# Kernel tuning notes

Measured on AMD Instinct MI355X. Metric: run time of the kernel, lower is better.

The kernel has to match this reference:

```python
import jax, jax.numpy as jnp
import numpy as np

NUM_HEADS = 8


def _forward(x, Wq, bq, Wk, bk, Wv, bv, Wo, bo, w1, b1, w2, b2, tau):
    B, S, E = x.shape
    H = NUM_HEADS
    hd = E // H
    scale = hd ** -0.5

    def heads(t):
        return t.reshape(B, S, H, hd).transpose(0, 2, 1, 3)  # [B,H,S,hd]

    q = heads(x @ Wq + bq)
    k = heads(x @ Wk + bk)
    v = heads(x @ Wv + bv)
    s = jnp.einsum('bhqd,bhkd->bhqk', q, k) * scale  # [B,H,S,S]

    # ---- autopoietic transform (vectorized over batch, no mask) ----
    s = jnp.clip(jnp.nan_to_num(s, nan=0.0, posinf=10.0, neginf=-10.0), -15.0, 15.0)
    ma = s.mean(axis=1)  # mean over heads -> [B,S,S]
    eps_safe = 0.05  # clamp(eps=1e-6, 0.05, 0.8)
    sa = jnp.clip(jnp.clip(ma, -8.0, 8.0) * eps_safe, -10.0, 10.0)
    # 1x1 conv on [1,1,S,S] == per-channel scalar scale+bias -> [B,C,S,S]
    hid = jax.nn.relu(jnp.clip(sa[:, None] * w1[None, :, None, None]
                               + b1[None, :, None, None], -5.0, 5.0))
    ap = jnp.clip(jnp.einsum('bcij,c->bij', hid, w2) + b2, -5.0, 5.0)
    taylor = jnp.clip(1.0 + 0.05 * (ap * 50.0), 0.5, 1.5)
    sig = jax.nn.sigmoid(taylor)
    p = jax.nn.softmax(jnp.clip(ma, -10.0, 10.0), axis=-1)
    Hent = -p * jnp.log(p + 1e-6)
    Fm = jax.nn.softmax(3.0 * Hent, axis=-1)
    t = sig * Fm
    eo = jnp.sqrt((ma * ma).sum(axis=(1, 2), keepdims=True)) + 1e-4  # fro norm
    et = jnp.sqrt((t * t).sum(axis=(1, 2), keepdims=True)) + 1e-4
    t = jnp.clip(eo / et, 0.8, 1.2) * t
    tm = t.mean(axis=(1, 2), keepdims=True)
    om = ma.mean(axis=(1, 2), keepdims=True)
    tstd = jnp.sqrt(jnp.clip(((t - tm) ** 2).mean(axis=(1, 2), keepdims=True), 0.01, None))
    ostd = jnp.sqrt(jnp.clip(((ma - om) ** 2).mean(axis=(1, 2), keepdims=True), 0.01, None))
    gd = jnp.clip(ostd / tstd, 0.8, 1.2)
    ar = jnp.clip(jnp.abs(ma).max(axis=(1, 2), keepdims=True), 1.0, 10.0)
    sm = jnp.clip(0.3 / jnp.log1p(ar), 0.1, 0.5)
    st = tm + sm * gd * (t - tm)  # scaled_transform
    ent = Hent.mean(axis=(1, 2), keepdims=True)
    ne = ent / jnp.log(jnp.float32(S))  # normalized entropy (max_entropy = log S)
    rr = 0.4 * (1.0 - jnp.clip(ne, 0.0, 0.4))  # residual ratio (base 0.4, entropy-damped)
    # blend transform back into per-head scores (res_scale = 1.0)
    s = s + rr[:, None] * (st - ma)[:, None]

    attn = jax.nn.softmax(s / tau, axis=-1)
    out = jnp.einsum('bhqk,bhkd->bhqd', attn, v)
    out = out.transpose(0, 2, 1, 3).reshape(B, S, E)
    return out @ Wo + bo


def setup_inputs() -> dict:
    key = jax.random.key(0)
    ks = jax.random.split(key, 8)
    B, S, E, C = 4, 512, 512, 128
    w_scale = 0.02
    return {
        'x': jax.random.normal(ks[0], (B, S, E), dtype=jnp.float32),
        'Wq': jax.random.normal(ks[1], (E, E), dtype=jnp.float32) * w_scale,
        'bq': jnp.zeros((E,), jnp.float32),
        'Wk': jax.random.normal(ks[2], (E, E), dtype=jnp.float32) * w_scale,
        'bk': jnp.zeros((E,), jnp.float32),
        'Wv': jax.random.normal(ks[3], (E, E), dtype=jnp.float32) * w_scale,
        'bv': jnp.zeros((E,), jnp.float32),
        'Wo': jax.random.normal(ks[4], (E, E), dtype=jnp.float32) * w_scale,
        'bo': jnp.zeros((E,), jnp.float32),
        'w1': jax.random.normal(ks[5], (C,), dtype=jnp.float32) * 0.5,
        'b1': jnp.zeros((C,), jnp.float32),
        'w2': jax.random.normal(ks[6], (C,), dtype=jnp.float32) * 0.1,
        'b2': jnp.zeros((1,), jnp.float32),
        'tau': jnp.ones((1,), jnp.float32),
    }


def reference(x, Wq, bq, Wk, bk, Wv, bv, Wo, bo, w1, b1, w2, b2, tau):
    return _forward(x, Wq, bq, Wk, bk, Wv, bv, Wo, bo, w1, b1, w2, b2, tau)
```

## Files before the change

kernel.cpp:

```cpp
#include <hip/hip_runtime.h>
#include <math.h>

#define BB 4
#define SS 512
#define EE 512
#define NH 8
#define HD 64
#define NC 128
#define NTAB 4096

typedef _Float16 f16x8 __attribute__((ext_vector_type(8)));
typedef float f32x4 __attribute__((ext_vector_type(4)));

struct HL { _Float16 h, l; };

__device__ __forceinline__ float clampf(float v, float lo, float hi) {
  return fminf(fmaxf(v, lo), hi);
}
__device__ __forceinline__ HL split16(float x) {
  HL r;
  r.h = (_Float16)x;
  r.l = (_Float16)(x - (float)r.h);
  return r;
}

__device__ __forceinline__ float waveRedSum(float v) {
#pragma unroll
  for (int o = 32; o; o >>= 1) v += __shfl_xor(v, o);
  return v;
}
__device__ __forceinline__ float waveRedMax(float v) {
#pragma unroll
  for (int o = 32; o; o >>= 1) v = fmaxf(v, __shfl_xor(v, o));
  return v;
}
__device__ __forceinline__ float blockRedSum(float v, float* red) {
  int tid = threadIdx.x;
  v = waveRedSum(v);
  __syncthreads();
  if ((tid & 63) == 0) red[tid >> 6] = v;
  __syncthreads();
  return red[0] + red[1] + red[2] + red[3];
}
__device__ __forceinline__ float blockRedMax(float v, float* red) {
  int tid = threadIdx.x;
  v = waveRedMax(v);
  __syncthreads();
  if ((tid & 63) == 0) red[tid >> 6] = v;
  __syncthreads();
  return fmaxf(fmaxf(red[0], red[1]), fmaxf(red[2], red[3]));
}

__global__ __launch_bounds__(256) void k_prep(
    const float* __restrict__ w1, const float* __restrict__ b1,
    const float* __restrict__ w2, const float* __restrict__ b2,
    float* __restrict__ T, const float* __restrict__ x,
    _Float16* __restrict__ xh, _Float16* __restrict__ xl,
    const float* __restrict__ Wq, const float* __restrict__ Wk,
    const float* __restrict__ Wv, const float* __restrict__ Wo,
    _Float16* __restrict__ Wth, _Float16* __restrict__ Wtl) {
  const int bid = blockIdx.x;
  const int tid = threadIdx.x;
  if (bid < 17) {
    int idx = bid * 256 + tid;
    if (idx > NTAB) return;
    float sa = -0.4f + (float)idx * (0.8f / (float)NTAB);
    float ap = 0.f;
#pragma unroll 4
    for (int c = 0; c < NC; ++c) {
      float h = fminf(fmaxf(sa * w1[c] + b1[c], 0.f), 5.f);
      ap += h * w2[c];
    }
    ap = clampf(ap + b2[0], -5.f, 5.f);
    float tay = clampf(1.0f + 0.05f * (ap * 50.0f), 0.5f, 1.5f);
    T[idx] = 1.0f / (1.0f + expf(-tay));
  } else if (bid < 529) {
    int idx = ((bid - 17) * 256 + tid) * 8;
    float4 u0 = *(const float4*)(x + idx);
    float4 u1 = *(const float4*)(x + idx + 4);
    float f[8] = {u0.x, u0.y, u0.z, u0.w, u1.x, u1.y, u1.z, u1.w};
    f16x8 h, l;
#pragma unroll
    for (int j = 0; j < 8; ++j) {
      HL r = split16(f[j]);
      h[j] = r.h;
      l[j] = r.l;
    }
    *(f16x8*)(xh + idx) = h;
    *(f16x8*)(xl + idx) = l;
  } else {
    const int j = bid - 529;
    const int z = j >> 6;
    const int rem = j & 63;
    const int k0 = (rem & 7) * 64, n0 = (rem >> 3) * 64;
    const float* W = (z == 0) ? Wq : (z == 1) ? Wk : (z == 2) ? Wv : Wo;
    __shared__ float Tt[64][68];
    const int r = tid >> 2, c = (tid & 3) * 16;
#pragma unroll
    for (int jj = 0; jj < 16; jj += 4)
      *(float4*)&Tt[r][c + jj] =
          *(const float4*)(W + (size_t)(k0 + r) * EE + n0 + c + jj);
    __syncthreads();
    f16x8 h0, l0, h1, l1;
#pragma unroll
    for (int jj = 0; jj < 8; ++jj) {
      HL r0 = split16(Tt[c + jj][r]);
      HL r1 = split16(Tt[c + 8 + jj][r]);
      h0[jj] = r0.h; l0[jj] = r0.l;
      h1[jj] = r1.h; l1[jj] = r1.l;
    }
    _Float16* dh = Wth + ((size_t)z * EE + n0 + r) * EE + k0 + c;
    _Float16* dl = Wtl + ((size_t)z * EE + n0 + r) * EE + k0 + c;
    *(f16x8*)dh = h0;
    *(f16x8*)(dh + 8) = h1;
    *(f16x8*)dl = l0;
    *(f16x8*)(dl + 8) = l1;
  }
}

__global__ __launch_bounds__(256) void k_qkv_mfma(
    const _Float16* __restrict__ xh, const _Float16* __restrict__ xl,
    const _Float16* __restrict__ Wth, const _Float16* __restrict__ Wtl,
    const float* __restrict__ bq, const float* __restrict__ bk,
    const float* __restrict__ bv,
    _Float16* __restrict__ qh, _Float16* __restrict__ ql,
    _Float16* __restrict__ kh, _Float16* __restrict__ kl,
    _Float16* __restrict__ vth, _Float16* __restrict__ vtl) {
  const int which = blockIdx.z;
  const int tid = threadIdx.x;
  const int wave = tid >> 6, lane = tid & 63;
  const int quad = lane >> 4, l16 = lane & 15;
  const int m0 = blockIdx.y * 64;
  const int n0 = blockIdx.x * 64;
  const _Float16* Bh = Wth + (size_t)which * EE * EE;
  const _Float16* Bl = Wtl + (size_t)which * EE * EE;

  __shared__ __align__(16) char smpool[36864];
  _Float16(*LAh)[72] = (_Float16(*)[72])(smpool);
  _Float16(*LAl)[72] = (_Float16(*)[72])(smpool + 9216);
  _Float16(*LBh)[72] = (_Float16(*)[72])(smpool + 18432);
  _Float16(*LBl)[72] = (_Float16(*)[72])(smpool + 27648);
  float(*TR)[68] = (float(*)[68])(smpool);

  const int sr0 = tid >> 3, sc0 = (tid & 7) * 8;
  const int sr1 = (tid + 256) >> 3, sc1 = sc0;

  f32x4 acc[4] = {};
  for (int k0 = 0; k0 < EE; k0 += 64) {
    if (k0) __syncthreads();
    *(f16x8*)&LAh[sr0][sc0] = *(const f16x8*)(xh + (size_t)(m0 + sr0) * EE + k0 + sc0);
    *(f16x8*)&LAl[sr0][sc0] = *(const f16x8*)(xl + (size_t)(m0 + sr0) * EE + k0 + sc0);
    *(f16x8*)&LBh[sr0][sc0] = *(const f16x8*)(Bh + (size_t)(n0 + sr0) * EE + k0 + sc0);
    *(f16x8*)&LBl[sr0][sc0] = *(const f16x8*)(Bl + (size_t)(n0 + sr0) * EE + k0 + sc0);
    *(f16x8*)&LAh[sr1][sc1] = *(const f16x8*)(xh + (size_t)(m0 + sr1) * EE + k0 + sc1);
    *(f16x8*)&LAl[sr1][sc1] = *(const f16x8*)(xl + (size_t)(m0 + sr1) * EE + k0 + sc1);
    *(f16x8*)&LBh[sr1][sc1] = *(const f16x8*)(Bh + (size_t)(n0 + sr1) * EE + k0 + sc1);
    *(f16x8*)&LBl[sr1][sc1] = *(const f16x8*)(Bl + (size_t)(n0 + sr1) * EE + k0 + sc1);
    __syncthreads();
#pragma unroll
    for (int kk = 0; kk < 64; kk += 32) {
      f16x8 ah = *(const f16x8*)&LAh[wave * 16 + l16][kk + quad * 8];
      f16x8 al = *(const f16x8*)&LAl[wave * 16 + l16][kk + quad * 8];
#pragma unroll
      for (int nt = 0; nt < 4; ++nt) {
        f16x8 bhf = *(const f16x8*)&LBh[nt * 16 + l16][kk + quad * 8];
        f16x8 blf = *(const f16x8*)&LBl[nt * 16 + l16][kk + quad * 8];
        acc[nt] = __builtin_amdgcn_mfma_f32_16x16x32_f16(ah, bhf, acc[nt], 0, 0, 0);
        acc[nt] = __builtin_amdgcn_mfma_f32_16x16x32_f16(ah, blf, acc[nt], 0, 0, 0);
        acc[nt] = __builtin_amdgcn_mfma_f32_16x16x32_f16(al, bhf, acc[nt], 0, 0, 0);
      }
    }
  }
  const float* bias = (which == 0) ? bq : (which == 1) ? bk : bv;
  if (which == 2) {
    __syncthreads();
#pragma unroll
    for (int nt = 0; nt < 4; ++nt) {
      const int dcol = nt * 16 + l16;
      const float bb = bias[n0 + nt * 16 + l16];
#pragma unroll
      for (int r = 0; r < 4; ++r)
        TR[dcol][wave * 16 + quad * 4 + r] = acc[nt][r] + bb;
    }
    __syncthreads();
    const int d = tid >> 2, cc = (tid & 3) * 16;
    const int bh = (m0 >> 9) * NH + (n0 >> 6);
    const int si0 = m0 & 511;
    f16x8 h0, l0, h1, l1;
#pragma unroll
    for (int jj = 0; jj < 8; ++jj) {
      HL r0 = split16(TR[d][cc + jj]);
      HL r1 = split16(TR[d][cc + 8 + jj]);
      h0[jj] = r0.h; l0[jj] = r0.l;
      h1[jj] = r1.h; l1[jj] = r1.l;
    }
    _Float16* dh = vth + ((size_t)bh * HD + d) * SS + si0 + cc;
    _Float16* dl = vtl + ((size_t)bh * HD + d) * SS + si0 + cc;
    *(f16x8*)dh = h0;
    *(f16x8*)(dh + 8) = h1;
    *(f16x8*)dl = l0;
    *(f16x8*)(dl + 8) = l1;
  } else {
    const float postscale = (which == 0) ? 0.125f : 1.0f;
    const int mbase = m0 + wave * 16 + quad * 4;
#pragma unroll
    for (int nt = 0; nt < 4; ++nt) {
      const int col = n0 + nt * 16 + l16;
      const float bb = bias[col];
      const int hh = col >> 6, d = col & 63;
#pragma unroll
      for (int r = 0; r < 4; ++r) {
        const int mm = mbase + r;
        const int b_ = mm >> 9, si = mm & 511;
        const size_t idx = (((size_t)(b_ * NH + hh)) * SS + si) * HD + d;
        const float val = (acc[nt][r] + bb) * postscale;
        HL sp = split16(val);
        (which ? kh : qh)[idx] = sp.h;
        (which ? kl : ql)[idx] = sp.l;
      }
    }
  }
}

__global__ __launch_bounds__(256) void k_scores_mfma(
    const _Float16* __restrict__ qh, const _Float16* __restrict__ ql,
    const _Float16* __restrict__ kh, const _Float16* __restrict__ kl,
    float* __restrict__ s) {
  const int bh = blockIdx.z;
  const int i0 = blockIdx.y * 64, j0 = blockIdx.x * 64;
  const int tid = threadIdx.x;
  const int wave = tid >> 6, lane = tid & 63;
  const int quad = lane >> 4, l16 = lane & 15;

  __shared__ _Float16 Qh[64][72], Ql[64][72], Kh[64][72], Kl[64][72];
  const int r = tid >> 2, c = (tid & 3) * 16;
  {
    const size_t qoff = ((size_t)bh * SS + i0 + r) * HD + c;
    const size_t koff = ((size_t)bh * SS + j0 + r) * HD + c;
    *(f16x8*)&Qh[r][c] = *(const f16x8*)(qh + qoff);
    *(f16x8*)&Qh[r][c + 8] = *(const f16x8*)(qh + qoff + 8);
    *(f16x8*)&Ql[r][c] = *(const f16x8*)(ql + qoff);
    *(f16x8*)&Ql[r][c + 8] = *(const f16x8*)(ql + qoff + 8);
    *(f16x8*)&Kh[r][c] = *(const f16x8*)(kh + koff);
    *(f16x8*)&Kh[r][c + 8] = *(const f16x8*)(kh + koff + 8);
    *(f16x8*)&Kl[r][c] = *(const f16x8*)(kl + koff);
    *(f16x8*)&Kl[r][c + 8] = *(const f16x8*)(kl + koff + 8);
  }
  __syncthreads();

  f16x8 a_hi[2], a_lo[2];
#pragma unroll
  for (int ks = 0; ks < 2; ++ks) {
    a_hi[ks] = *(const f16x8*)&Qh[wave * 16 + l16][ks * 32 + quad * 8];
    a_lo[ks] = *(const f16x8*)&Ql[wave * 16 + l16][ks * 32 + quad * 8];
  }
  f32x4 acc[4] = {};
#pragma unroll
  for (int ks = 0; ks < 2; ++ks) {
#pragma unroll
    for (int t = 0; t < 4; ++t) {
      f16x8 b_hi = *(const f16x8*)&Kh[t * 16 + l16][ks * 32 + quad * 8];
      f16x8 b_lo = *(const f16x8*)&Kl[t * 16 + l16][ks * 32 + quad * 8];
      acc[t] = __builtin_amdgcn_mfma_f32_16x16x32_f16(a_hi[ks], b_hi,
                                                      acc[t], 0, 0, 0);
      acc[t] = __builtin_amdgcn_mfma_f32_16x16x32_f16(a_hi[ks], b_lo,
                                                      acc[t], 0, 0, 0);
      acc[t] = __builtin_amdgcn_mfma_f32_16x16x32_f16(a_lo[ks], b_hi,
                                                      acc[t], 0, 0, 0);
    }
  }
  float* sb = s + (size_t)bh * SS * SS;
#pragma unroll
  for (int t = 0; t < 4; ++t) {
#pragma unroll
    for (int r2 = 0; r2 < 4; ++r2) {
      float val = clampf(acc[t][r2], -15.0f, 15.0f);
      sb[(size_t)(i0 + wave * 16 + quad * 4 + r2) * SS + j0 + t * 16 + l16] = val;
    }
  }
}

__global__ __launch_bounds__(64) void k_rowstat(
    const float* __restrict__ s, const float* __restrict__ T,
    float* __restrict__ ma, float* __restrict__ t_un,
    float* __restrict__ rowred) {
  const int row = blockIdx.x;
  const int b_ = row >> 9, i = row & 511;
  const int lane = threadIdx.x;

  float4 a0 = {0.f, 0.f, 0.f, 0.f}, a1 = {0.f, 0.f, 0.f, 0.f};
#pragma unroll
  for (int hh = 0; hh < NH; ++hh) {
    const float4* p = reinterpret_cast<const float4*>(
                          s + (((size_t)(b_ * NH + hh) * SS) + i) * SS) +
                      lane * 2;
    float4 u0 = p[0], u1 = p[1];
    a0.x += u0.x; a0.y += u0.y; a0.z += u0.z; a0.w += u0.w;
    a1.x += u1.x; a1.y += u1.y; a1.z += u1.z; a1.w += u1.w;
  }
  float m[8] = {a0.x * 0.125f, a0.y * 0.125f, a0.z * 0.125f, a0.w * 0.125f,
                a1.x * 0.125f, a1.y * 0.125f, a1.z * 0.125f, a1.w * 0.125f};
  {
    float4* mp = reinterpret_cast<float4*>(ma + ((size_t)b_ * SS + i) * SS) +
                 lane * 2;
    float4 w0 = {m[0], m[1], m[2], m[3]}, w1v = {m[4], m[5], m[6], m[7]};
    mp[0] = w0;
    mp[1] = w1v;
  }
  float sma = 0.f, sma2 = 0.f, mabs = 0.f;
#pragma unroll
  for (int e = 0; e < 8; ++e) {
    sma += m[e];
    sma2 += m[e] * m[e];
    mabs = fmaxf(mabs, fabsf(m[e]));
  }
  sma = waveRedSum(sma);
  sma2 = waveRedSum(sma2);
  mabs = waveRedMax(mabs);

  float ex[8], esum = 0.f;
#pragma unroll
  for (int e = 0; e < 8; ++e) {
    ex[e] = expf(clampf(m[e], -10.f, 10.f));
    esum += ex[e];
  }
  esum = waveRedSum(esum);
  float inv = 1.0f / esum;
  float Hv[8], sH = 0.f;
#pragma unroll
  for (int e = 0; e < 8; ++e) {
    float p = ex[e] * inv;
    Hv[e] = -p * logf(p + 1e-6f);
    sH += Hv[e];
  }
  sH = waveRedSum(sH);

  float fx[8], fsum = 0.f;
#pragma unroll
  for (int e = 0; e < 8; ++e) {
    fx[e] = expf(3.0f * Hv[e]);
    fsum += fx[e];
  }
  fsum = waveRedSum(fsum);
  float finv = 1.0f / fsum;

  float t[8], st = 0.f, st2 = 0.f;
#pragma unroll
  for (int e = 0; e < 8; ++e) {
    float sa = clampf(m[e], -8.f, 8.f) * 0.05f;
    float pos = (sa + 0.4f) * ((float)NTAB / 0.8f);
    int idx = (int)pos;
    idx = idx < 0 ? 0 : (idx > NTAB - 1 ? NTAB - 1 : idx);
    float frac = pos - (float)idx;
    float g0 = T[idx], g1 = T[idx + 1];
    float sig = g0 + (g1 - g0) * frac;
    t[e] = sig * fx[e] * finv;
    st += t[e];
    st2 += t[e] * t[e];
  }
  st = waveRedSum(st);
  st2 = waveRedSum(st2);
  {
    float4* tp = reinterpret_cast<float4*>(t_un + ((size_t)b_ * SS + i) * SS) +
                 lane * 2;
    float4 w0 = {t[0], t[1], t[2], t[3]}, w1v = {t[4], t[5], t[6], t[7]};
    tp[0] = w0;
    tp[1] = w1v;
  }
  if (lane == 0) {
    float* rp = rowred + (size_t)row * 8;
    rp[0] = sma; rp[1] = sma2; rp[2] = mabs;
    rp[3] = st;  rp[4] = st2;  rp[5] = sH;
  }
}

__global__ __launch_bounds__(256) void k_consts(
    const float* __restrict__ rowred, float* __restrict__ cst) {
  const int b_ = blockIdx.x;
  const int tid = threadIdx.x;
  __shared__ float red[4];
  const float* r0 = rowred + ((size_t)b_ * SS + tid * 2) * 8;
  const float* r1 = r0 + 8;
  float sma = blockRedSum(r0[0] + r1[0], red);
  float sma2 = blockRedSum(r0[1] + r1[1], red);
  float mabs = blockRedMax(fmaxf(r0[2], r1[2]), red);
  float st = blockRedSum(r0[3] + r1[3], red);
  float st2 = blockRedSum(r0[4] + r1[4], red);
  float sH = blockRedSum(r0[5] + r1[5], red);
  if (tid == 0) {
    const float N = (float)(SS * SS);
    float eo = sqrtf(sma2) + 1e-4f;
    float et = sqrtf(st2) + 1e-4f;
    float r = clampf(eo / et, 0.8f, 1.2f);
    float tmean = r * st / N;
    float om = sma / N;
    float vart = r * r * fmaxf(st2 / N - (st / N) * (st / N), 0.f);
    float tstd = sqrtf(fmaxf(vart, 0.01f));
    float varo = fmaxf(sma2 / N - om * om, 0.f);
    float ostd = sqrtf(fmaxf(varo, 0.01f));
    float gd = clampf(ostd / tstd, 0.8f, 1.2f);
    float ar = clampf(mabs, 1.f, 10.f);
    float sm = clampf(0.3f / log1pf(ar), 0.1f, 0.5f);
    float ent = sH / N;
    float ne = ent / logf((float)SS);
    float rr = 0.4f * (1.f - clampf(ne, 0.f, 0.4f));
    float G = sm * gd;
    cst[b_ * 4 + 0] = rr * (1.f - G) * tmean;
    cst[b_ * 4 + 1] = rr * G * r;
    cst[b_ * 4 + 2] = rr;
  }
}

__global__ __launch_bounds__(64) void k_blend(
    const float* __restrict__ s, const float* __restrict__ ma,
    const float* __restrict__ t_un, const float* __restrict__ cst,
    const float* __restrict__ tau, _Float16* __restrict__ ph,
    _Float16* __restrict__ pl) {
  const int rid = blockIdx.x;
  const int bh = rid >> 9, i = rid & 511;
  const int b_ = bh >> 3;
  const int lane = threadIdx.x;
  const float c0 = cst[b_ * 4 + 0], c1 = cst[b_ * 4 + 1], c2 = cst[b_ * 4 + 2];
  const float itau = 1.0f / tau[0];
  const size_t rowbase = ((size_t)bh * SS + i) * SS;
  const float* srow = s + rowbase;
  const float* mrow = ma + ((size_t)b_ * SS + i) * SS;
  const float* trow = t_un + ((size_t)b_ * SS + i) * SS;

  float e[8], sum = 0.f;
#pragma unroll
  for (int u = 0; u < 2; ++u) {
    float4 sv = ((const float4*)srow)[lane * 2 + u];
    float4 mv = ((const float4*)mrow)[lane * 2 + u];
    float4 tv = ((const float4*)trow)[lane * 2 + u];
    const float* sp = (const float*)&sv;
    const float* mp = (const float*)&mv;
    const float* tp = (const float*)&tv;
#pragma unroll
    for (int j = 0; j < 4; ++j) {
      float vv = (sp[j] + c0 + c1 * tp[j] - c2 * mp[j]) * itau;
      e[u * 4 + j] = expf(vv);
      sum += e[u * 4 + j];
    }
  }
  sum = waveRedSum(sum);
  const float inv = 1.0f / sum;
  f16x8 hv, lv;
#pragma unroll
  for (int j = 0; j < 8; ++j) {
    HL r = split16(e[j] * inv);
    hv[j] = r.h;
    lv[j] = r.l;
  }
  *(f16x8*)(ph + rowbase + lane * 8) = hv;
  *(f16x8*)(pl + rowbase + lane * 8) = lv;
}

__global__ __launch_bounds__(256) void k_av_mfma(
    const _Float16* __restrict__ ph, const _Float16* __restrict__ pl,
    const _Float16* __restrict__ vth, const _Float16* __restrict__ vtl,
    _Float16* __restrict__ oh, _Float16* __restrict__ ol) {
  const int bh = blockIdx.y;
  const int b_ = bh >> 3, hh = bh & 7;
  const int m0 = blockIdx.x * 64;
  const int tid = threadIdx.x;
  const int wave = tid >> 6, lane = tid & 63;
  const int quad = lane >> 4, l16 = lane & 15;

  __shared__ _Float16 Ph[64][40], Pl[64][40];
  const int srow = tid >> 2, schunk = (tid & 3) * 8;
  const size_t pbase = ((size_t)bh * SS + m0 + srow) * SS + schunk;

  f16x8 rh = *(const f16x8*)(ph + pbase);
  f16x8 rl = *(const f16x8*)(pl + pbase);

  f32x4 acc[4] = {};
  for (int k0 = 0; k0 < SS; k0 += 32) {
    if (k0) __syncthreads();
    *(f16x8*)&Ph[srow][schunk] = rh;
    *(f16x8*)&Pl[srow][schunk] = rl;
    __syncthreads();
    if (k0 + 32 < SS) {
      rh = *(const f16x8*)(ph + pbase + k0 + 32);
      rl = *(const f16x8*)(pl + pbase + k0 + 32);
    }
    const size_t boff = ((size_t)bh * HD + wave * 16 + l16) * SS + k0 + quad * 8;
    f16x8 bh_ = *(const f16x8*)(vth + boff);
    f16x8 bl_ = *(const f16x8*)(vtl + boff);
#pragma unroll
    for (int mt = 0; mt < 4; ++mt) {
      f16x8 ah = *(const f16x8*)&Ph[mt * 16 + l16][quad * 8];
      f16x8 al = *(const f16x8*)&Pl[mt * 16 + l16][quad * 8];
      acc[mt] = __builtin_amdgcn_mfma_f32_16x16x32_f16(ah, bh_, acc[mt], 0, 0, 0);
      acc[mt] = __builtin_amdgcn_mfma_f32_16x16x32_f16(ah, bl_, acc[mt], 0, 0, 0);
      acc[mt] = __builtin_amdgcn_mfma_f32_16x16x32_f16(al, bh_, acc[mt], 0, 0, 0);
    }
  }
#pragma unroll
  for (int mt = 0; mt < 4; ++mt) {
#pragma unroll
    for (int r = 0; r < 4; ++r) {
      const int si = m0 + mt * 16 + quad * 4 + r;
      const size_t idx =
          ((size_t)(b_ * SS + si)) * EE + hh * HD + wave * 16 + l16;
      HL sp = split16(acc[mt][r]);
      oh[idx] = sp.h;
      ol[idx] = sp.l;
    }
  }
}

__global__ __launch_bounds__(256) void k_out_mfma(
    const _Float16* __restrict__ oh, const _Float16* __restrict__ ol,
    const _Float16* __restrict__ Wth, const _Float16* __restrict__ Wtl,
    const float* __restrict__ bo, float* __restrict__ out) {
  const int tid = threadIdx.x;
  const int wave = tid >> 6, lane = tid & 63;
  const int quad = lane >> 4, l16 = lane & 15;
  const int m0 = blockIdx.y * 64;
  const int n0 = blockIdx.x * 64;
  const _Float16* Bh = Wth + (size_t)3 * EE * EE;
  const _Float16* Bl = Wtl + (size_t)3 * EE * EE;

  __shared__ _Float16 LAh[64][72], LAl[64][72], LBh[64][72], LBl[64][72];

  const int sr0 = tid >> 3, sc0 = (tid & 7) * 8;
  const int sr1 = (tid + 256) >> 3, sc1 = sc0;

  f32x4 acc[4] = {};
  for (int k0 = 0; k0 < EE; k0 += 64) {
    if (k0) __syncthreads();
    *(f16x8*)&LAh[sr0][sc0] = *(const f16x8*)(oh + (size_t)(m0 + sr0) * EE + k0 + sc0);
    *(f16x8*)&LAl[sr0][sc0] = *(const f16x8*)(ol + (size_t)(m0 + sr0) * EE + k0 + sc0);
    *(f16x8*)&LBh[sr0][sc0] = *(const f16x8*)(Bh + (size_t)(n0 + sr0) * EE + k0 + sc0);
    *(f16x8*)&LBl[sr0][sc0] = *(const f16x8*)(Bl + (size_t)(n0 + sr0) * EE + k0 + sc0);
    *(f16x8*)&LAh[sr1][sc1] = *(const f16x8*)(oh + (size_t)(m0 + sr1) * EE + k0 + sc1);
    *(f16x8*)&LAl[sr1][sc1] = *(const f16x8*)(ol + (size_t)(m0 + sr1) * EE + k0 + sc1);
    *(f16x8*)&LBh[sr1][sc1] = *(const f16x8*)(Bh + (size_t)(n0 + sr1) * EE + k0 + sc1);
    *(f16x8*)&LBl[sr1][sc1] = *(const f16x8*)(Bl + (size_t)(n0 + sr1) * EE + k0 + sc1);
    __syncthreads();
#pragma unroll
    for (int kk = 0; kk < 64; kk += 32) {
      f16x8 ah = *(const f16x8*)&LAh[wave * 16 + l16][kk + quad * 8];
      f16x8 al = *(const f16x8*)&LAl[wave * 16 + l16][kk + quad * 8];
#pragma unroll
      for (int nt = 0; nt < 4; ++nt) {
        f16x8 bhf = *(const f16x8*)&LBh[nt * 16 + l16][kk + quad * 8];
        f16x8 blf = *(const f16x8*)&LBl[nt * 16 + l16][kk + quad * 8];
        acc[nt] = __builtin_amdgcn_mfma_f32_16x16x32_f16(ah, bhf, acc[nt], 0, 0, 0);
        acc[nt] = __builtin_amdgcn_mfma_f32_16x16x32_f16(ah, blf, acc[nt], 0, 0, 0);
        acc[nt] = __builtin_amdgcn_mfma_f32_16x16x32_f16(al, bhf, acc[nt], 0, 0, 0);
      }
    }
  }
  const int mbase = m0 + wave * 16 + quad * 4;
#pragma unroll
  for (int nt = 0; nt < 4; ++nt) {
    const int col = n0 + nt * 16 + l16;
    const float bb = bo[col];
#pragma unroll
    for (int r = 0; r < 4; ++r) {
      const int m = mbase + r;
      out[(size_t)m * EE + col] = acc[nt][r] + bb;
    }
  }
}

extern "C" void kernel_launch(void* const* d_in, const int* in_sizes, int n_in,
                              void* d_out, int out_size, void* d_ws,
                              size_t ws_size, hipStream_t stream) {
  const float* x = (const float*)d_in[0];
  const float* Wq = (const float*)d_in[1];
  const float* bq = (const float*)d_in[2];
  const float* Wk = (const float*)d_in[3];
  const float* bk = (const float*)d_in[4];
  const float* Wv = (const float*)d_in[5];
  const float* bv = (const float*)d_in[6];
  const float* Wo = (const float*)d_in[7];
  const float* bo = (const float*)d_in[8];
  const float* w1 = (const float*)d_in[9];
  const float* b1 = (const float*)d_in[10];
  const float* w2 = (const float*)d_in[11];
  const float* b2 = (const float*)d_in[12];
  const float* tau = (const float*)d_in[13];
  float* out = (float*)d_out;

  const size_t NX = (size_t)2048 * EE;
  const size_t NW = (size_t)4 * EE * EE;
  const size_t NQK = (size_t)BB * NH * SS * HD;
  const size_t NS = (size_t)BB * NH * SS * SS;

  _Float16* xh = (_Float16*)d_ws;
  _Float16* xl = xh + NX;
  _Float16* Wth = xl + NX;
  _Float16* Wtl = Wth + NW;
  _Float16* qh = Wtl + NW;
  _Float16* ql = qh + NQK;
  _Float16* kh = ql + NQK;
  _Float16* kl = kh + NQK;
  _Float16* vth = kl + NQK;
  _Float16* vtl = vth + NQK;
  float* s = (float*)(vtl + NQK);
  float* ma = s + NS;
  float* t_un = ma + (size_t)BB * SS * SS;
  float* T = t_un + (size_t)BB * SS * SS;
  float* rowred = T + 8192;
  float* cst = rowred + 2048 * 8;
  _Float16* ph = (_Float16*)(cst + 16);
  _Float16* pl = ph + NS;
  _Float16* oh = xh;
  _Float16* ol = xl;

  k_prep<<<785, 256, 0, stream>>>(w1, b1, w2, b2, T, x, xh, xl, Wq, Wk, Wv, Wo,
                                  Wth, Wtl);
  k_qkv_mfma<<<dim3(8, 32, 3), 256, 0, stream>>>(xh, xl, Wth, Wtl, bq, bk, bv,
                                                 qh, ql, kh, kl, vth, vtl);
  k_scores_mfma<<<dim3(8, 8, 32), 256, 0, stream>>>(qh, ql, kh, kl, s);
  k_rowstat<<<2048, 64, 0, stream>>>(s, T, ma, t_un, rowred);
  k_consts<<<4, 256, 0, stream>>>(rowred, cst);
  k_blend<<<16384, 64, 0, stream>>>(s, ma, t_un, cst, tau, ph, pl);
  k_av_mfma<<<dim3(8, 32), 256, 0, stream>>>(ph, pl, vth, vtl, oh, ol);
  k_out_mfma<<<dim3(8, 32), 256, 0, stream>>>(oh, ol, Wth, Wtl, bo, out);
}
```

Measured before the change: 171.3 us.

## Fuse softmax blend into AV matmul with deferred normalization

Drops the separate blend kernel, which wrote fp16 hi/lo probability matrices, and computes the unnormalized exponentials inside the AV MFMA kernel while loading each K-tile. Row sums are accumulated per thread, reduced through shared memory, and applied as a divide on the output. This avoids a full write and read of the two B*H*S*S fp16 probability buffers. The cost is that each tile now loads three fp32 inputs and runs exp on the critical path, and there is no max-subtraction. Only a fixed 2^-16 prescale guards against fp16 overflow.

Result: no change. 170.5 us (-0.5%).

```diff
diff --git a/kernel.cpp b/kernel.cpp
--- a/kernel.cpp
+++ b/kernel.cpp
@@ -411,55 +411,12 @@
   }
 }
 
-__global__ __launch_bounds__(64) void k_blend(
+__global__ __launch_bounds__(256) void k_av_fused(
     const float* __restrict__ s, const float* __restrict__ ma,
     const float* __restrict__ t_un, const float* __restrict__ cst,
-    const float* __restrict__ tau, _Float16* __restrict__ ph,
-    _Float16* __restrict__ pl) {
-  const int rid = blockIdx.x;
-  const int bh = rid >> 9, i = rid & 511;
-  const int b_ = bh >> 3;
-  const int lane = threadIdx.x;
-  const float c0 = cst[b_ * 4 + 0], c1 = cst[b_ * 4 + 1], c2 = cst[b_ * 4 + 2];
-  const float itau = 1.0f / tau[0];
-  const size_t rowbase = ((size_t)bh * SS + i) * SS;
-  const float* srow = s + rowbase;
-  const float* mrow = ma + ((size_t)b_ * SS + i) * SS;
-  const float* trow = t_un + ((size_t)b_ * SS + i) * SS;
-
-  float e[8], sum = 0.f;
-#pragma unroll
-  for (int u = 0; u < 2; ++u) {
-    float4 sv = ((const float4*)srow)[lane * 2 + u];
-    float4 mv = ((const float4*)mrow)[lane * 2 + u];
-    float4 tv = ((const float4*)trow)[lane * 2 + u];
-    const float* sp = (const float*)&sv;
-    const float* mp = (const float*)&mv;
-    const float* tp = (const float*)&tv;
-#pragma unroll
-    for (int j = 0; j < 4; ++j) {
-      float vv = (sp[j] + c0 + c1 * tp[j] - c2 * mp[j]) * itau;
-      e[u * 4 + j] = expf(vv);
-      sum += e[u * 4 + j];
-    }
-  }
-  sum = waveRedSum(sum);
-  const float inv = 1.0f / sum;
-  f16x8 hv, lv;
-#pragma unroll
-  for (int j = 0; j < 8; ++j) {
-    HL r = split16(e[j] * inv);
-    hv[j] = r.h;
-    lv[j] = r.l;
-  }
-  *(f16x8*)(ph + rowbase + lane * 8) = hv;
-  *(f16x8*)(pl + rowbase + lane * 8) = lv;
-}
-
-__global__ __launch_bounds__(256) void k_av_mfma(
-    const _Float16* __restrict__ ph, const _Float16* __restrict__ pl,
-    const _Float16* __restrict__ vth, const _Float16* __restrict__ vtl,
-    _Float16* __restrict__ oh, _Float16* __restrict__ ol) {
+    const float* __restrict__ tau, const _Float16* __restrict__ vth,
+    const _Float16* __restrict__ vtl, _Float16* __restrict__ oh,
+    _Float16* __restrict__ ol) {
   const int bh = blockIdx.y;
   const int b_ = bh >> 3, hh = bh & 7;
   const int m0 = blockIdx.x * 64;
@@ -467,22 +424,54 @@
   const int wave = tid >> 6, lane = tid & 63;
   const int quad = lane >> 4, l16 = lane & 15;
 
+  const float c0 = cst[b_ * 4 + 0], c1 = cst[b_ * 4 + 1], c2 = cst[b_ * 4 + 2];
+  const float itau = 1.0f / tau[0];
+
   __shared__ _Float16 Ph[64][40], Pl[64][40];
-  const int srow = tid >> 2, schunk = (tid & 3) * 8;
-  const size_t pbase = ((size_t)bh * SS + m0 + srow) * SS + schunk;
-
-  f16x8 rh = *(const f16x8*)(ph + pbase);
-  f16x8 rl = *(const f16x8*)(pl + pbase);
-
+  __shared__ float Zp[64][4];
+
+  const int srow = tid >> 2;
+  const int ci = tid & 3;
+  const int schunk = ci * 8;
+  const size_t sbase = ((size_t)bh * SS + m0 + srow) * SS + schunk;
+  const size_t mbase = ((size_t)b_ * SS + m0 + srow) * SS + schunk;
+
+  float4 sv0 = *(const float4*)(s + sbase);
+  float4 sv1 = *(const float4*)(s + sbase + 4);
+  float4 mv0 = *(const float4*)(ma + mbase);
+  float4 mv1 = *(const float4*)(ma + mbase + 4);
+  float4 tv0 = *(const float4*)(t_un + mbase);
+  float4 tv1 = *(const float4*)(t_un + mbase + 4);
+
+  float zpart = 0.f;
   f32x4 acc[4] = {};
   for (int k0 = 0; k0 < SS; k0 += 32) {
     if (k0) __syncthreads();
-    *(f16x8*)&Ph[srow][schunk] = rh;
-    *(f16x8*)&Pl[srow][schunk] = rl;
+    {
+      float svv[8] = {sv0.x, sv0.y, sv0.z, sv0.w, sv1.x, sv1.y, sv1.z, sv1.w};
+      float mvv[8] = {mv0.x, mv0.y, mv0.z, mv0.w, mv1.x, mv1.y, mv1.z, mv1.w};
+      float tvv[8] = {tv0.x, tv0.y, tv0.z, tv0.w, tv1.x, tv1.y, tv1.z, tv1.w};
+      f16x8 hv, lv;
+#pragma unroll
+      for (int j = 0; j < 8; ++j) {
+        float vv = (svv[j] + c0 + c1 * tvv[j] - c2 * mvv[j]) * itau;
+        float e = expf(vv) * 1.52587890625e-05f;
+        zpart += e;
+        HL r = split16(e);
+        hv[j] = r.h;
+        lv[j] = r.l;
+      }
+      *(f16x8*)&Ph[srow][schunk] = hv;
+      *(f16x8*)&Pl[srow][schunk] = lv;
+    }
     __syncthreads();
     if (k0 + 32 < SS) {
-      rh = *(const f16x8*)(ph + pbase + k0 + 32);
-      rl = *(const f16x8*)(pl + pbase + k0 + 32);
+      sv0 = *(const float4*)(s + sbase + k0 + 32);
+      sv1 = *(const float4*)(s + sbase + k0 + 36);
+      mv0 = *(const float4*)(ma + mbase + k0 + 32);
+      mv1 = *(const float4*)(ma + mbase + k0 + 36);
+      tv0 = *(const float4*)(t_un + mbase + k0 + 32);
+      tv1 = *(const float4*)(t_un + mbase + k0 + 36);
     }
     const size_t boff = ((size_t)bh * HD + wave * 16 + l16) * SS + k0 + quad * 8;
     f16x8 bh_ = *(const f16x8*)(vth + boff);
@@ -496,14 +485,20 @@
       acc[mt] = __builtin_amdgcn_mfma_f32_16x16x32_f16(al, bh_, acc[mt], 0, 0, 0);
     }
   }
+  __syncthreads();
+  Zp[srow][ci] = zpart;
+  __syncthreads();
 #pragma unroll
   for (int mt = 0; mt < 4; ++mt) {
 #pragma unroll
     for (int r = 0; r < 4; ++r) {
-      const int si = m0 + mt * 16 + quad * 4 + r;
+      const int lr = mt * 16 + quad * 4 + r;
+      const float Z = Zp[lr][0] + Zp[lr][1] + Zp[lr][2] + Zp[lr][3];
+      const float oV = acc[mt][r] / Z;
+      const int si = m0 + lr;
       const size_t idx =
           ((size_t)(b_ * SS + si)) * EE + hh * HD + wave * 16 + l16;
-      HL sp = split16(acc[mt][r]);
+      HL sp = split16(oV);
       oh[idx] = sp.h;
       ol[idx] = sp.l;
     }
@@ -606,8 +601,6 @@
   float* T = t_un + (size_t)BB * SS * SS;
   float* rowred = T + 8192;
   float* cst = rowred + 2048 * 8;
-  _Float16* ph = (_Float16*)(cst + 16);
-  _Float16* pl = ph + NS;
   _Float16* oh = xh;
   _Float16* ol = xl;
 
@@ -618,7 +611,7 @@
   k_scores_mfma<<<dim3(8, 8, 32), 256, 0, stream>>>(qh, ql, kh, kl, s);
   k_rowstat<<<2048, 64, 0, stream>>>(s, T, ma, t_un, rowred);
   k_consts<<<4, 256, 0, stream>>>(rowred, cst);
-  k_blend<<<16384, 64, 0, stream>>>(s, ma, t_un, cst, tau, ph, pl);
-  k_av_mfma<<<dim3(8, 32), 256, 0, stream>>>(ph, pl, vth, vtl, oh, ol);
+  k_av_fused<<<dim3(8, 32), 256, 0, stream>>>(s, ma, t_un, cst, tau, vth, vtl,
+                                              oh, ol);
   k_out_mfma<<<dim3(8, 32), 256, 0, stream>>>(oh, ol, Wth, Wtl, bo, out);
 }
```
